# Optimization experiments

Measured on AMD Instinct MI355X. Metric: run time of the kernel, lower is better.

Reference implementation:

```python
import jax, jax.numpy as jnp
import numpy as np

N_E = 16384
E_DIM = 64
GROUPS = 4
N_E_GROUP = N_E // GROUPS  # 4096
B, H, W = 16, 32, 32


def _l2norm(x):
    # matches F.normalize(p=2, dim=-1) with eps=1e-12
    n = jnp.linalg.norm(x, axis=-1, keepdims=True)
    return x / jnp.maximum(n, 1e-12)


def setup_inputs() -> dict:
    key = jax.random.key(0)
    k1, k2 = jax.random.split(key)
    z_groups = jax.random.normal(k1, (B, GROUPS * E_DIM, H, W), dtype=jnp.float32)
    emb = jax.random.uniform(k2, (N_E, E_DIM), minval=-1.0 / N_E, maxval=1.0 / N_E,
                             dtype=jnp.float32)
    emb = _l2norm(emb)  # module normalizes codebook at init when l2_norm=True
    return {"z_groups": z_groups, "embedding": emb}


def reference(z_groups, embedding):
    # Eval-mode forward (no EMA/random-restart buffer updates, losses are 0).
    b, c, h, w = z_groups.shape
    # split channels into groups: b (g*c) h w -> b h w g c
    z = z_groups.reshape(b, GROUPS, E_DIM, h, w).transpose(0, 3, 4, 1, 2)
    z = _l2norm(z)                                     # l2_norm=True path
    zf = z.reshape(-1, GROUPS, E_DIM)                  # [N, g, c]
    emb = _l2norm(embedding.reshape(GROUPS, N_E_GROUP, E_DIM))  # [g, k, c]

    # d = -|z|^2 - |e|^2 + 2 z.e  (negative squared distance), argmax = nearest
    d = (2.0 * jnp.einsum('ngc,gkc->ngk', zf, emb)
         - jnp.sum(zf * zf, axis=-1)[..., None]
         - jnp.sum(emb * emb, axis=-1)[None, :, :])    # [N, g, k]
    idx = jnp.argmax(d, axis=-1)                       # [N, g]

    zq = emb[jnp.arange(GROUPS)[None, :], idx]         # [N, g, c] gather
    zq = zf + jax.lax.stop_gradient(zq - zf)           # straight-through

    # b h w g c -> b (g*c) h w
    quant = zq.reshape(b, h, w, GROUPS, E_DIM).transpose(0, 3, 4, 1, 2)
    quant = quant.reshape(b, GROUPS * E_DIM, h, w)

    vq_loss = jnp.zeros((GROUPS,), jnp.float32)
    commit_loss = jnp.zeros((GROUPS,), jnp.float32)
    codebook_usage = jnp.zeros((GROUPS,), jnp.float32)

    # perplexity / min_encodings correspond to the last group (loop semantics)
    min_encodings = jax.nn.one_hot(idx[:, -1], N_E_GROUP, dtype=quant.dtype)
    avg_probs = jnp.mean(min_encodings, axis=0)
    perplexity = jnp.exp(-jnp.sum(avg_probs * jnp.log(avg_probs + 1e-10)))

    return (quant, vq_loss, commit_loss, codebook_usage,
            perplexity, min_encodings, idx)
```

## Files before the change

kernel.cpp:

```cpp
#include <hip/hip_runtime.h>
#include <hip/hip_bf16.h>
#include <math.h>

#define N_E      16384
#define E_DIM    64
#define GROUPS   4
#define N_E_G    4096
#define NQ       16384

#define OFF_QUANT   0L
#define OFF_VQLOSS  4194304L
#define OFF_PERP    4194316L
#define OFF_MINENC  4194317L
#define OFF_IDX     71303181L

#define WS_EN     0L
#define WS_EN2    1048576L
#define WS_ENHI   1064960L
#define WS_ZNR    1589248L
#define WS_ZHI    5783552L
#define WS_HIST   7880704L
#define WS_IDX3   7884800L

typedef float  float4v  __attribute__((ext_vector_type(4)));
typedef short  short8   __attribute__((ext_vector_type(8)));

static __device__ __forceinline__ ushort f2bf(float x) {
    union { __hip_bfloat16 h; ushort u; } cv; cv.h = __float2bfloat16(x);
    return cv.u;
}

__global__ void norm_all_kernel(const float* __restrict__ emb,
                                const float* __restrict__ z,
                                float* __restrict__ en, float* __restrict__ en2,
                                ushort* __restrict__ ehi,
                                float* __restrict__ znr, ushort* __restrict__ zhi) {
    __shared__ float tile[64 * 65];
    __shared__ float rden[64];
    const int t = threadIdx.x;

    if (blockIdx.x < 4096) {
        int gid  = blockIdx.x * 256 + t;
        int code = gid >> 6;
        int lane = t & 63;
        float x = emb[code * 64 + lane];
        float ss = x * x;
        #pragma unroll
        for (int off = 32; off; off >>= 1) ss += __shfl_xor(ss, off, 64);
        float v = x / fmaxf(sqrtf(ss), 1e-12f);
        en[code * 64 + lane]  = v;
        ehi[code * 64 + lane] = f2bf(v);
        float s2 = v * v;
        #pragma unroll
        for (int off = 32; off; off >>= 1) s2 += __shfl_xor(s2, off, 64);
        if (lane == 0) en2[code] = s2;
        return;
    }

    int bx2 = blockIdx.x - 4096;
    int g   = bx2 >> 8;
    int n0  = (bx2 & 255) * 64;
    int b   = n0 >> 10, hw0 = n0 & 1023;
    const float* src = z + (size_t)b * 262144 + (size_t)g * 65536 + hw0;

    for (int i = t; i < 4096; i += 256) {
        int d = i >> 6, nl = i & 63;
        tile[d * 65 + nl] = src[(size_t)d * 1024 + nl];
    }
    __syncthreads();

    if (t < 64) {
        float ss = 0.f;
        for (int d = 0; d < 64; ++d) {
            float x = tile[d * 65 + t];
            ss = fmaf(x, x, ss);
        }
        rden[t] = fmaxf(sqrtf(ss), 1e-12f);
    }
    __syncthreads();

    for (int i = t; i < 4096; i += 256) {
        int q = i >> 6, d = i & 63;
        float v = tile[d * 65 + q] / rden[q];
        size_t o = ((size_t)g * NQ + n0 + q) * 64 + d;
        znr[o] = v;
        zhi[o] = f2bf(v);
    }
}

#define CAP  64
#define TAU  0.017f
__global__ __launch_bounds__(256, 2)
void vq_cand_kernel(const ushort* __restrict__ zhi, const ushort* __restrict__ ehi,
                    const float* __restrict__ znr, const float* __restrict__ en,
                    const float* __restrict__ en2, float* __restrict__ out,
                    int* __restrict__ hist, int* __restrict__ idx3) {
    __shared__ int    cnt[128];
    __shared__ ushort cand[128 * CAP];
    __shared__ int    bks[128];

    const int g  = blockIdx.y;
    const int q0 = blockIdx.x * 128;
    const int t  = threadIdx.x;
    const int wave = t >> 6, lane = t & 63;
    const int l15 = lane & 15, quad = lane >> 4;
    const int qhalf = wave & 1, chalf = wave >> 1;

    const int sliceId = blockIdx.y * (NQ / 128) + blockIdx.x;
    float4v* fill4 = (float4v*)(out + OFF_VQLOSS) + (size_t)sliceId * 32768;

    if (t < 128) cnt[t] = 0;

    short8 bfrag[4][2];
    {
        const ushort* zq = zhi + ((size_t)g * NQ + q0 + qhalf * 64 + l15) * 64 + quad * 8;
        #pragma unroll
        for (int u = 0; u < 4; ++u)
            #pragma unroll
            for (int ks = 0; ks < 2; ++ks)
                bfrag[u][ks] = *(const short8*)(zq + u * 16 * 64 + ks * 32);
    }
    __syncthreads();

    const ushort* abase = ehi + (size_t)g * N_E_G * 64
                        + (size_t)(chalf * 64 + l15) * 64 + quad * 8;

    float Mrun[4];
    #pragma unroll
    for (int u = 0; u < 4; ++u) Mrun[u] = -3.4e38f;

    short8 afA[4][2], afB[4][2];
    #pragma unroll
    for (int cs = 0; cs < 4; ++cs)
        #pragma unroll
        for (int ks = 0; ks < 2; ++ks)
            afA[cs][ks] = *(const short8*)(abase + (size_t)(cs * 16) * 64 + ks * 32);

    auto do_tile = [&](short8 (&A)[4][2], short8 (&P)[4][2], int tile) {
        if (tile + 1 < 32) {
            const ushort* p = abase + (size_t)((tile + 1) * 128) * 64;
            #pragma unroll
            for (int cs = 0; cs < 4; ++cs)
                #pragma unroll
                for (int ks = 0; ks < 2; ++ks)
                    P[cs][ks] = *(const short8*)(p + (size_t)(cs * 16) * 64 + ks * 32);
        }
        {
            const float4v z4 = {0.f, 0.f, 0.f, 0.f};
            #pragma unroll
            for (int r = 0; r < 4; ++r)
                fill4[(size_t)(tile * 4 + r) * 256 + t] = z4;
        }
        float4v acc[4][4];
        #pragma unroll
        for (int cs = 0; cs < 4; ++cs)
            #pragma unroll
            for (int u = 0; u < 4; ++u) {
                float4v zz = {0.f, 0.f, 0.f, 0.f};
                float4v tmp = __builtin_amdgcn_mfma_f32_16x16x32_bf16(
                                  A[cs][0], bfrag[u][0], zz, 0, 0, 0);
                acc[cs][u] = __builtin_amdgcn_mfma_f32_16x16x32_bf16(
                                  A[cs][1], bfrag[u][1], tmp, 0, 0, 0);
            }
        const int j0 = tile * 128;
        #pragma unroll
        for (int u = 0; u < 4; ++u) {
            float m = acc[0][u][0];
            #pragma unroll
            for (int cs = 0; cs < 4; ++cs)
                #pragma unroll
                for (int r = 0; r < 4; ++r) m = fmaxf(m, acc[cs][u][r]);
            float m2 = fmaxf(m, __shfl_xor(m, 16, 64));
            float m4 = fmaxf(m2, __shfl_xor(m2, 32, 64));
            Mrun[u] = fmaxf(Mrun[u], m4);
            float thr = Mrun[u] - TAU;
            if (m >= thr) {
                int ql = qhalf * 64 + u * 16 + l15;
                #pragma unroll
                for (int cs = 0; cs < 4; ++cs)
                    #pragma unroll
                    for (int r = 0; r < 4; ++r)
                        if (acc[cs][u][r] >= thr) {
                            int cidx = j0 + chalf * 64 + cs * 16 + quad * 4 + r;
                            int slot = atomicAdd(&cnt[ql], 1);
                            if (slot < CAP) cand[ql * CAP + slot] = (ushort)cidx;
                        }
            }
        }
    };

    for (int tt = 0; tt < 32; tt += 2) {
        do_tile(afA, afB, tt);
        do_tile(afB, afA, tt + 1);
    }

    if (sliceId == 0 && t < 13) out[OFF_VQLOSS + 67108864L + t] = 0.f;
    __syncthreads();

    if (t < 128) {
        int q = q0 + t;
        float za[64];
        const float4v* zp = (const float4v*)(znr + ((size_t)g * NQ + q) * 64);
        #pragma unroll
        for (int i = 0; i < 16; ++i) {
            float4v v = zp[i];
            za[i*4+0] = v[0]; za[i*4+1] = v[1]; za[i*4+2] = v[2]; za[i*4+3] = v[3];
        }
        int nc = cnt[t]; if (nc > CAP) nc = CAP;
        float best = -3.4e38f; int bk = 0x7fffffff;
        for (int s = 0; s < nc; ++s) {
            int c = cand[t * CAP + s];
            const float* ev = en + ((size_t)g * N_E_G + c) * 64;
            float a = 0.f;
            #pragma unroll
            for (int k = 0; k < 64; ++k) a = fmaf(za[k], ev[k], a);
            float d = 2.f * a - en2[g * N_E_G + c];
            if (d > best || (d == best && c < bk)) { best = d; bk = c; }
        }
        if (bk == 0x7fffffff) bk = 0;
        bks[t] = bk;
        out[OFF_IDX + (size_t)q * 4 + g] = (float)bk;
        if (g == 3) {
            idx3[q] = bk;
            atomicAdd(&hist[bk], 1);
        }
    }
    __syncthreads();

    for (int i = t; i < 128 * 64; i += 256) {
        int d = i >> 7, m = i & 127;
        int n = q0 + m, b = n >> 10, hw = n & 1023;
        out[OFF_QUANT + (size_t)b * 262144 + (size_t)(g * 64 + d) * 1024 + hw] =
            en[((size_t)g * N_E_G + bks[m]) * 64 + d];
    }
}

__global__ void finalize_kernel(const int* __restrict__ idx3,
                                const int* __restrict__ hist,
                                float* __restrict__ out) {
    if (blockIdx.x < 64) {
        int r = blockIdx.x * 256 + threadIdx.x;
        out[OFF_MINENC + (size_t)r * N_E_G + idx3[r]] = 1.0f;
        return;
    }
    __shared__ float s[256];
    int t = threadIdx.x;
    float acc = 0.f;
    for (int k = t; k < N_E_G; k += 256) {
        float p = (float)hist[k] * (1.0f / 16384.0f);
        acc += p * logf(p + 1e-10f);
    }
    s[t] = acc;
    __syncthreads();
    for (int o = 128; o; o >>= 1) {
        if (t < o) s[t] += s[t + o];
        __syncthreads();
    }
    if (t == 0) out[OFF_PERP] = expf(-s[0]);
}

extern "C" void kernel_launch(void* const* d_in, const int* in_sizes, int n_in,
                              void* d_out, int out_size, void* d_ws, size_t ws_size,
                              hipStream_t stream) {
    const float* z_groups = (const float*)d_in[0];
    const float* emb      = (const float*)d_in[1];
    float* out = (float*)d_out;
    float* ws  = (float*)d_ws;

    float*  en   = ws + WS_EN;
    float*  en2  = ws + WS_EN2;
    ushort* ehi  = (ushort*)(ws + WS_ENHI);
    float*  znr  = ws + WS_ZNR;
    ushort* zhi  = (ushort*)(ws + WS_ZHI);
    int*    hist = (int*)(ws + WS_HIST);
    int*    idx3 = (int*)(ws + WS_IDX3);

    hipMemsetAsync(hist, 0, N_E_G * sizeof(int), stream);

    norm_all_kernel<<<4096 + 1024, 256, 0, stream>>>(emb, z_groups,
                                                     en, en2, ehi, znr, zhi);

    vq_cand_kernel<<<dim3(NQ / 128, GROUPS), 256, 0, stream>>>(
        zhi, ehi, znr, en, en2, out, hist, idx3);

    finalize_kernel<<<65, 256, 0, stream>>>(idx3, hist, out);
}
```

Measured before the change: 402.5 us.

## Halve queries per block, raise occupancy, drop prefetch, fold hist memset into norm kernel

The candidate kernel now handles 64 queries per block instead of 128, doubling the grid to 256x4 blocks. Launch bounds rise to 4 blocks per SM, and the double-buffered codebook prefetch is replaced by a simple per-tile load. The aim is more latency hiding through occupancy and better load balance. The cost is that each codebook tile is read twice as often across blocks and in-register prefetch is lost. The hist memset is moved into an extra block of the normalization kernel, removing a separate memset launch.

```diff
diff --git a/kernel.cpp b/kernel.cpp
--- a/kernel.cpp
+++ b/kernel.cpp
@@ -34,26 +34,32 @@
                                 const float* __restrict__ z,
                                 float* __restrict__ en, float* __restrict__ en2,
                                 ushort* __restrict__ ehi,
-                                float* __restrict__ znr, ushort* __restrict__ zhi) {
+                                float* __restrict__ znr, ushort* __restrict__ zhi,
+                                int* __restrict__ hist) {
     __shared__ float tile[64 * 65];
     __shared__ float rden[64];
     const int t = threadIdx.x;
 
+    if (blockIdx.x == 4096 + 1024) {
+        for (int i = t; i < N_E_G; i += 256) hist[i] = 0;
+        return;
+    }
+
     if (blockIdx.x < 4096) {
         int gid  = blockIdx.x * 256 + t;
         int code = gid >> 6;
-        int lane = t & 63;
-        float x = emb[code * 64 + lane];
+        int k    = t & 63;
+        float x = emb[code * 64 + k];
         float ss = x * x;
         #pragma unroll
         for (int off = 32; off; off >>= 1) ss += __shfl_xor(ss, off, 64);
         float v = x / fmaxf(sqrtf(ss), 1e-12f);
-        en[code * 64 + lane]  = v;
-        ehi[code * 64 + lane] = f2bf(v);
+        en[code * 64 + k]  = v;
+        ehi[code * 64 + k] = f2bf(v);
         float s2 = v * v;
         #pragma unroll
         for (int off = 32; off; off >>= 1) s2 += __shfl_xor(s2, off, 64);
-        if (lane == 0) en2[code] = s2;
+        if (k == 0) en2[code] = s2;
         return;
     }
 
@@ -90,81 +96,72 @@
 
 #define CAP  64
 #define TAU  0.017f
-__global__ __launch_bounds__(256, 2)
+__global__ __launch_bounds__(256, 4)
 void vq_cand_kernel(const ushort* __restrict__ zhi, const ushort* __restrict__ ehi,
                     const float* __restrict__ znr, const float* __restrict__ en,
                     const float* __restrict__ en2, float* __restrict__ out,
                     int* __restrict__ hist, int* __restrict__ idx3) {
-    __shared__ int    cnt[128];
-    __shared__ ushort cand[128 * CAP];
-    __shared__ int    bks[128];
+    __shared__ int    cnt[64];
+    __shared__ ushort cand[64 * CAP];
+    __shared__ int    bks[64];
 
     const int g  = blockIdx.y;
-    const int q0 = blockIdx.x * 128;
+    const int q0 = blockIdx.x * 64;
     const int t  = threadIdx.x;
     const int wave = t >> 6, lane = t & 63;
     const int l15 = lane & 15, quad = lane >> 4;
     const int qhalf = wave & 1, chalf = wave >> 1;
 
-    const int sliceId = blockIdx.y * (NQ / 128) + blockIdx.x;
-    float4v* fill4 = (float4v*)(out + OFF_VQLOSS) + (size_t)sliceId * 32768;
-
-    if (t < 128) cnt[t] = 0;
-
-    short8 bfrag[4][2];
-    {
-        const ushort* zq = zhi + ((size_t)g * NQ + q0 + qhalf * 64 + l15) * 64 + quad * 8;
-        #pragma unroll
-        for (int u = 0; u < 4; ++u)
-            #pragma unroll
-            for (int ks = 0; ks < 2; ++ks)
-                bfrag[u][ks] = *(const short8*)(zq + u * 16 * 64 + ks * 32);
-    }
+    const int sliceId = g * 256 + blockIdx.x;
+    float4v* fill4 = (float4v*)(out + OFF_VQLOSS) + (size_t)sliceId * 16384;
+    const float4v z4 = {0.f, 0.f, 0.f, 0.f};
+
+    if (t < 64) cnt[t] = 0;
+
+    short8 bfrag[2][2];
+    #pragma unroll
+    for (int u = 0; u < 2; ++u)
+        #pragma unroll
+        for (int ks = 0; ks < 2; ++ks)
+            bfrag[u][ks] = *(const short8*)(zhi +
+                ((size_t)g * NQ + q0 + qhalf * 32 + u * 16 + l15) * 64
+                + ks * 32 + quad * 8);
     __syncthreads();
 
     const ushort* abase = ehi + (size_t)g * N_E_G * 64
                         + (size_t)(chalf * 64 + l15) * 64 + quad * 8;
 
-    float Mrun[4];
-    #pragma unroll
-    for (int u = 0; u < 4; ++u) Mrun[u] = -3.4e38f;
-
-    short8 afA[4][2], afB[4][2];
-    #pragma unroll
-    for (int cs = 0; cs < 4; ++cs)
-        #pragma unroll
-        for (int ks = 0; ks < 2; ++ks)
-            afA[cs][ks] = *(const short8*)(abase + (size_t)(cs * 16) * 64 + ks * 32);
-
-    auto do_tile = [&](short8 (&A)[4][2], short8 (&P)[4][2], int tile) {
-        if (tile + 1 < 32) {
-            const ushort* p = abase + (size_t)((tile + 1) * 128) * 64;
+    float Mrun[2];
+    Mrun[0] = -3.4e38f; Mrun[1] = -3.4e38f;
+
+    for (int tile = 0; tile < 32; ++tile) {
+        short8 af[4][2];
+        {
+            const ushort* p = abase + (size_t)(tile * 128) * 64;
             #pragma unroll
             for (int cs = 0; cs < 4; ++cs)
                 #pragma unroll
                 for (int ks = 0; ks < 2; ++ks)
-                    P[cs][ks] = *(const short8*)(p + (size_t)(cs * 16) * 64 + ks * 32);
-        }
-        {
-            const float4v z4 = {0.f, 0.f, 0.f, 0.f};
-            #pragma unroll
-            for (int r = 0; r < 4; ++r)
-                fill4[(size_t)(tile * 4 + r) * 256 + t] = z4;
-        }
-        float4v acc[4][4];
+                    af[cs][ks] = *(const short8*)(p + (size_t)(cs * 16) * 64 + ks * 32);
+        }
+        fill4[(size_t)(tile * 2 + 0) * 256 + t] = z4;
+        fill4[(size_t)(tile * 2 + 1) * 256 + t] = z4;
+
+        float4v acc[4][2];
         #pragma unroll
         for (int cs = 0; cs < 4; ++cs)
             #pragma unroll
-            for (int u = 0; u < 4; ++u) {
+            for (int u = 0; u < 2; ++u) {
                 float4v zz = {0.f, 0.f, 0.f, 0.f};
                 float4v tmp = __builtin_amdgcn_mfma_f32_16x16x32_bf16(
-                                  A[cs][0], bfrag[u][0], zz, 0, 0, 0);
+                                  af[cs][0], bfrag[u][0], zz, 0, 0, 0);
                 acc[cs][u] = __builtin_amdgcn_mfma_f32_16x16x32_bf16(
-                                  A[cs][1], bfrag[u][1], tmp, 0, 0, 0);
+                                  af[cs][1], bfrag[u][1], tmp, 0, 0, 0);
             }
+
         const int j0 = tile * 128;
         #pragma unroll
-        for (int u = 0; u < 4; ++u) {
+        for (int u = 0; u < 2; ++u) {
             float m = acc[0][u][0];
             #pragma unroll
             for (int cs = 0; cs < 4; ++cs)
@@ -175,7 +172,7 @@
             Mrun[u] = fmaxf(Mrun[u], m4);
             float thr = Mrun[u] - TAU;
             if (m >= thr) {
-                int ql = qhalf * 64 + u * 16 + l15;
+                int ql = qhalf * 32 + u * 16 + l15;
                 #pragma unroll
                 for (int cs = 0; cs < 4; ++cs)
                     #pragma unroll
@@ -187,17 +184,12 @@
                         }
             }
         }
-    };
-
-    for (int tt = 0; tt < 32; tt += 2) {
-        do_tile(afA, afB, tt);
-        do_tile(afB, afA, tt + 1);
     }
 
     if (sliceId == 0 && t < 13) out[OFF_VQLOSS + 67108864L + t] = 0.f;
     __syncthreads();
 
-    if (t < 128) {
+    if (t < 64) {
         int q = q0 + t;
         float za[64];
         const float4v* zp = (const float4v*)(znr + ((size_t)g * NQ + q) * 64);
@@ -227,8 +219,8 @@
     }
     __syncthreads();
 
-    for (int i = t; i < 128 * 64; i += 256) {
-        int d = i >> 7, m = i & 127;
+    for (int i = t; i < 64 * 64; i += 256) {
+        int d = i >> 6, m = i & 63;
         int n = q0 + m, b = n >> 10, hw = n & 1023;
         out[OFF_QUANT + (size_t)b * 262144 + (size_t)(g * 64 + d) * 1024 + hw] =
             en[((size_t)g * N_E_G + bks[m]) * 64 + d];
@@ -275,12 +267,10 @@
     int*    hist = (int*)(ws + WS_HIST);
     int*    idx3 = (int*)(ws + WS_IDX3);
 
-    hipMemsetAsync(hist, 0, N_E_G * sizeof(int), stream);
-
-    norm_all_kernel<<<4096 + 1024, 256, 0, stream>>>(emb, z_groups,
-                                                     en, en2, ehi, znr, zhi);
-
-    vq_cand_kernel<<<dim3(NQ / 128, GROUPS), 256, 0, stream>>>(
+    norm_all_kernel<<<4096 + 1024 + 1, 256, 0, stream>>>(
+        emb, z_groups, en, en2, ehi, znr, zhi, hist);
+
+    vq_cand_kernel<<<dim3(256, GROUPS), 256, 0, stream>>>(
         zhi, ehi, znr, en, en2, out, hist, idx3);
 
     finalize_kernel<<<65, 256, 0, stream>>>(idx3, hist, out);
```

Result: slower. 447.1 us (+11.1%).
